# Optimization experiments

Hardware: AMD Instinct MI355X
Metric: run time of the kernel (lower is better)

The kernel has to match this reference:

```python
import jax, jax.numpy as jnp
import numpy as np
import math

D_MODEL = 1024
N_HEADS = 16
HEAD_DIM = D_MODEL // N_HEADS
SEQ = 2048
BATCH = 4
MAX_SEQ_LEN = 2048
THETA = 10000.0


def setup_inputs() -> dict:
    key = jax.random.key(0)
    ks = jax.random.split(key, 5)
    std = math.sqrt(2.0 / (D_MODEL + D_MODEL))
    x = jax.random.normal(ks[0], (BATCH, SEQ, D_MODEL), dtype=jnp.float32)
    wq = jax.random.normal(ks[1], (D_MODEL, D_MODEL), dtype=jnp.float32) * std
    wk = jax.random.normal(ks[2], (D_MODEL, D_MODEL), dtype=jnp.float32) * std
    wv = jax.random.normal(ks[3], (D_MODEL, D_MODEL), dtype=jnp.float32) * std
    wo = jax.random.normal(ks[4], (D_MODEL, D_MODEL), dtype=jnp.float32) * std
    token_positions = jnp.arange(SEQ, dtype=jnp.int32)
    return {"x": x, "token_positions": token_positions,
            "wq": wq, "wk": wk, "wv": wv, "wo": wo}


def _rope_tables(token_positions):
    # thetas_i = 1 / theta^(2i/d_k), angles[p, i] = p * thetas_i
    thetas = 1.0 / (THETA ** (2.0 * jnp.arange(HEAD_DIM // 2, dtype=jnp.float32) / HEAD_DIM))
    positions = jnp.arange(MAX_SEQ_LEN, dtype=jnp.float32)
    angles = jnp.outer(positions, thetas)  # [max_seq, d_k/2]
    cos = jnp.cos(angles)[token_positions]  # [S, d_k/2]
    sin = jnp.sin(angles)[token_positions]
    return cos, sin


def _apply_rope(x, cos, sin):
    # x: [B, H, S, D]; pairs (even, odd) form complex numbers
    shp = x.shape
    x2 = x.reshape(*shp[:-1], HEAD_DIM // 2, 2)
    xe, xo = x2[..., 0], x2[..., 1]
    re = xe * cos - xo * sin
    im = xe * sin + xo * cos
    return jnp.stack([re, im], axis=-1).reshape(shp)


def reference(x, token_positions, wq, wk, wv, wo):
    B, S, _ = x.shape
    # LinearNoBias: einsum('...j,ij->...i', x, W)
    q = jnp.einsum('bsj,ij->bsi', x, wq)
    k = jnp.einsum('bsj,ij->bsi', x, wk)
    v = jnp.einsum('bsj,ij->bsi', x, wv)
    # split heads -> [B, H, S, D]
    q = q.reshape(B, S, N_HEADS, HEAD_DIM).transpose(0, 2, 1, 3)
    k = k.reshape(B, S, N_HEADS, HEAD_DIM).transpose(0, 2, 1, 3)
    v = v.reshape(B, S, N_HEADS, HEAD_DIM).transpose(0, 2, 1, 3)
    cos, sin = _rope_tables(token_positions)
    q = _apply_rope(q, cos, sin)
    k = _apply_rope(k, cos, sin)
    scores = jnp.einsum('bhqd,bhkd->bhqk', q, k) / math.sqrt(HEAD_DIM)
    causal = jnp.tril(jnp.ones((S, S), dtype=bool))
    scores = jnp.where(causal, scores, -jnp.inf)
    probs = jax.nn.softmax(scores, axis=-1)
    out = jnp.einsum('bhqk,bhkd->bhqd', probs, v)
    out = out.transpose(0, 2, 1, 3).reshape(B, S, N_HEADS * HEAD_DIM)
    return jnp.einsum('bsj,ij->bsi', out, wo)
```

## Files before the change

### kernel.cpp

```cpp
#include <hip/hip_runtime.h>
#include <stdint.h>

#define B_SZ 4
#define S_LEN 2048
#define NH 16
#define HD 64
#define DM 1024

typedef __bf16 bf16;
typedef __bf16 bf16x4 __attribute__((ext_vector_type(4)));
typedef __bf16 bf16x8 __attribute__((ext_vector_type(8)));
typedef float f32x4 __attribute__((ext_vector_type(4)));

#define MFMA16(a, b, c) __builtin_amdgcn_mfma_f32_16x16x32_bf16(a, b, c, 0, 0, 0)

__device__ __forceinline__ void gl2lds16(const void* g, void* l) {
  __builtin_amdgcn_global_load_lds(
      (__attribute__((address_space(1))) const void*)g,
      (__attribute__((address_space(3))) void*)l, 16, 0, 0);
}

__device__ __forceinline__ void bar_lgkm() {
  asm volatile("s_waitcnt lgkmcnt(0)\n\ts_barrier" ::: "memory");
}

__device__ __forceinline__ bf16x8 ldcvt(const float* p) {
  f32x4 u0 = *(const f32x4*)p;
  f32x4 u1 = *(const f32x4*)(p + 4);
  bf16x8 v;
#pragma unroll
  for (int j = 0; j < 4; j++) {
    v[j] = (bf16)u0[j];
    v[4 + j] = (bf16)u1[j];
  }
  return v;
}

__global__ void cvt_kernel(const float* __restrict__ x,
                           const float* __restrict__ wq,
                           const float* __restrict__ wk,
                           const float* __restrict__ wv,
                           const float* __restrict__ wo,
                           bf16* __restrict__ Xb, bf16* __restrict__ Wb,
                           long xN) {
  const long e = ((long)blockIdx.x * 256 + threadIdx.x) * 8;
  const float* src;
  bf16* dst;
  long off;
  if (e < xN) {
    src = x; dst = Xb; off = e;
  } else {
    const long w = e - xN;
    const int wi = (int)(w >> 20);
    src = (wi == 0) ? wq : (wi == 1) ? wk : (wi == 2) ? wv : wo;
    dst = Wb + ((size_t)wi << 20);
    off = w & ((1L << 20) - 1);
  }
  *(bf16x8*)(dst + off) = ldcvt(src + off);
}

__device__ __forceinline__ void gemm_core_bb(const bf16* __restrict__ Ag,
                                             const bf16* __restrict__ Bg,
                                             f32x4 acc[4][4], bf16* As,
                                             bf16* Bs) {
  const int tid = threadIdx.x;
  const int lane = tid & 63;
  const int wave = tid >> 6;
  const int wm = (wave >> 1) * 64;
  const int wn = (wave & 1) * 64;
  const int col = lane & 15;
  const int kq = (lane >> 4) * 8;
  const int r0 = tid >> 2;
  const int c0 = (tid & 3) * 8;
#pragma unroll
  for (int i = 0; i < 4; i++)
#pragma unroll
    for (int j = 0; j < 4; j++) acc[i][j] = (f32x4){0.f, 0.f, 0.f, 0.f};

  for (int k0 = 0; k0 < 1024; k0 += 32) {
    __syncthreads();
    gl2lds16(Ag + (size_t)r0 * 1024 + k0 + c0, As + tid * 8);
    gl2lds16(Ag + (size_t)(r0 + 64) * 1024 + k0 + c0, As + 2048 + tid * 8);
    gl2lds16(Bg + (size_t)r0 * 1024 + k0 + c0, Bs + tid * 8);
    gl2lds16(Bg + (size_t)(r0 + 64) * 1024 + k0 + c0, Bs + 2048 + tid * 8);
    __syncthreads();

    bf16x8 af[4], bfr[4];
#pragma unroll
    for (int i = 0; i < 4; i++)
      af[i] = *(const bf16x8*)(As + (wm + i * 16 + col) * 32 + kq);
#pragma unroll
    for (int j = 0; j < 4; j++)
      bfr[j] = *(const bf16x8*)(Bs + (wn + j * 16 + col) * 32 + kq);
#pragma unroll
    for (int i = 0; i < 4; i++)
#pragma unroll
      for (int j = 0; j < 4; j++)
        acc[i][j] = MFMA16(af[i], bfr[j], acc[i][j]);
  }
}

__global__ __launch_bounds__(256, 4) void qkv_gemm(
    const bf16* __restrict__ x, const bf16* __restrict__ Wb,
    bf16* __restrict__ Q, bf16* __restrict__ K, bf16* __restrict__ Vt) {
  __shared__ __align__(16) bf16 As[128 * 32];
  __shared__ __align__(16) bf16 Bs[128 * 32];
  const int bx = blockIdx.x;
  const int by = blockIdx.y;
  const int wsel = by >> 3;
  const int n0 = (by & 7) * 128;

  f32x4 acc[4][4];
  gemm_core_bb(x + (size_t)bx * 128 * 1024,
               Wb + ((size_t)wsel << 20) + (size_t)n0 * 1024, acc, As, Bs);

  const int lane = threadIdx.x & 63;
  const int wave = threadIdx.x >> 6;
  const int wm = (wave >> 1) * 64, wn = (wave & 1) * 64;
  const int col = lane & 15, quad = lane >> 4;

  if (wsel < 2) {
    bf16* dst = wsel ? K : Q;
#pragma unroll
    for (int i = 0; i < 4; i++) {
      const int m0 = bx * 128 + wm + i * 16 + quad * 4;
#pragma unroll
      for (int j = 0; j < 4; j++) {
        const int n = n0 + wn + j * 16 + col;
        const int h = n >> 6, d = n & 63;
#pragma unroll
        for (int r = 0; r < 4; r++) {
          const int mm = m0 + r;
          const int bl = mm >> 11, s = mm & 2047;
          dst[((((size_t)bl * NH + h) * S_LEN + s) << 6) + d] =
              (bf16)acc[i][j][r];
        }
      }
    }
  } else {
#pragma unroll
    for (int i = 0; i < 4; i++) {
      const int m0 = bx * 128 + wm + i * 16 + quad * 4;
      const int bl = m0 >> 11, s = m0 & 2047;
#pragma unroll
      for (int j = 0; j < 4; j++) {
        const int n = n0 + wn + j * 16 + col;
        const int h = n >> 6, d = n & 63;
        bf16x4 pk;
#pragma unroll
        for (int r = 0; r < 4; r++) pk[r] = (bf16)acc[i][j][r];
        *(bf16x4*)(Vt + (((size_t)(bl * NH + h) * 64 + d) << 11) + s) = pk;
      }
    }
  }
}

__global__ void rope_kernel(bf16* __restrict__ q, bf16* __restrict__ k,
                            const int* __restrict__ tp) {
  const float CS = 0.18033688011112042f;
  const int idx = blockIdx.x * 256 + threadIdx.x;
  const int srow = idx >> 3;
  const int d0 = (idx & 7) * 8;
  const int s = srow & (S_LEN - 1);
  const float pf = (float)tp[s];
  const int i0 = d0 >> 1;
  float cs[4], sn[4];
#pragma unroll
  for (int j = 0; j < 4; j++) {
    float freq = __builtin_exp2f(-(float)(i0 + j) * 0.41524101186091903f);
    float ang = pf * freq;
    sincosf(ang, &sn[j], &cs[j]);
  }
  const size_t off = (size_t)srow * 64 + d0;
  bf16x8 vq = *(bf16x8*)(q + off);
  bf16x8 vk = *(bf16x8*)(k + off);
#pragma unroll
  for (int j = 0; j < 4; j++) {
    float e = (float)vq[2 * j], o = (float)vq[2 * j + 1];
    vq[2 * j] = (bf16)((e * cs[j] - o * sn[j]) * CS);
    vq[2 * j + 1] = (bf16)((e * sn[j] + o * cs[j]) * CS);
    e = (float)vk[2 * j];
    o = (float)vk[2 * j + 1];
    vk[2 * j] = (bf16)(e * cs[j] - o * sn[j]);
    vk[2 * j + 1] = (bf16)(e * sn[j] + o * cs[j]);
  }
  *(bf16x8*)(q + off) = vq;
  *(bf16x8*)(k + off) = vk;
}

#define KP 72
#define VP 136
#define PP 72
__global__ __launch_bounds__(256, 2) void attn_kernel(
    const bf16* __restrict__ Q, const bf16* __restrict__ K,
    const bf16* __restrict__ Vt, bf16* __restrict__ O) {
  __shared__ __align__(16) bf16 Ks[128 * KP];
  __shared__ __align__(16) bf16 Vts[64 * VP];
  __shared__ __align__(16) bf16 Ps[4 * 64 * PP];

  const int tid = threadIdx.x, lane = tid & 63, wave = tid >> 6;
  const int col = lane & 15, quad = lane >> 4, kq = quad * 8;
  const int bh = blockIdx.x;
  const int yb = blockIdx.y;
  const int qt = (yb < 4) ? (7 - yb) : (yb - 4);
  const int bl = bh >> 4, h = bh & 15;
  const bf16* Kg = K + (size_t)bh * S_LEN * 64;
  const bf16* Vg = Vt + (size_t)bh * 64 * S_LEN;
  bf16* Pw = Ps + wave * 64 * PP;
  const int wq_abs = qt * 256 + wave * 64;
  const int qmax = wq_abs + 63;

  const bf16* Qg = Q + ((size_t)bh * S_LEN + wq_abs) * 64;
  bf16x8 qf[4][2];
#pragma unroll
  for (int mi = 0; mi < 4; mi++)
#pragma unroll
    for (int kc = 0; kc < 2; kc++)
      qf[mi][kc] =
          *(const bf16x8*)(Qg + (mi * 16 + col) * 64 + kc * 32 + kq);

  f32x4 oacc[4][4];
  float lst[4] = {0.f, 0.f, 0.f, 0.f};
#pragma unroll
  for (int mi = 0; mi < 4; mi++)
#pragma unroll
    for (int nd = 0; nd < 4; nd++) oacc[mi][nd] = (f32x4){0.f, 0.f, 0.f, 0.f};

  const int kiters = 2 * qt + 2;
  bf16x8 kreg[4], vreg[4];
#pragma unroll
  for (int p = 0; p < 4; p++) {
    const int g = p * 256 + tid;
    kreg[p] = *(const bf16x8*)(Kg + (size_t)(g >> 3) * 64 + (g & 7) * 8);
    vreg[p] = *(const bf16x8*)(Vg + (size_t)(g >> 4) * S_LEN + (g & 15) * 8);
  }

  for (int kt = 0; kt < kiters; kt++) {
    bar_lgkm();
#pragma unroll
    for (int p = 0; p < 4; p++) {
      const int g = p * 256 + tid;
      *(bf16x8*)(Ks + (g >> 3) * KP + (g & 7) * 8) = kreg[p];
      *(bf16x8*)(Vts + (g >> 4) * VP + (g & 15) * 8) = vreg[p];
    }
    if (kt + 1 < kiters) {
#pragma unroll
      for (int p = 0; p < 4; p++) {
        const int g = p * 256 + tid;
        kreg[p] = *(const bf16x8*)(Kg + (size_t)((kt + 1) * 128 + (g >> 3)) * 64 +
                                   (g & 7) * 8);
        vreg[p] = *(const bf16x8*)(Vg + (size_t)(g >> 4) * S_LEN +
                                   (kt + 1) * 128 + (g & 15) * 8);
      }
    }
    bar_lgkm();
    if (kt * 128 > qmax) continue;

#pragma unroll
    for (int hf = 0; hf < 2; hf++) {
      const int kb = kt * 128 + hf * 64;
      if (kb > qmax) break;
      f32x4 sa[4][4];
#pragma unroll
      for (int ni = 0; ni < 4; ni++) {
        const int krow = hf * 64 + ni * 16 + col;
        bf16x8 kf0 = *(const bf16x8*)(Ks + krow * KP + kq);
        bf16x8 kf1 = *(const bf16x8*)(Ks + krow * KP + 32 + kq);
#pragma unroll
        for (int mi = 0; mi < 4; mi++) {
          f32x4 s = {0.f, 0.f, 0.f, 0.f};
          s = MFMA16(kf0, qf[mi][0], s);
          s = MFMA16(kf1, qf[mi][1], s);
          sa[mi][ni] = s;
        }
      }
      if (kb + 63 > wq_abs) {
        const int base = kb - wq_abs + quad * 4;
#pragma unroll
        for (int mi = 0; mi < 4; mi++)
#pragma unroll
          for (int ni = 0; ni < 4; ni++)
#pragma unroll
            for (int r = 0; r < 4; r++)
              if (base + ni * 16 + r > mi * 16 + col) sa[mi][ni][r] = -1e30f;
      }
#pragma unroll
      for (int mi = 0; mi < 4; mi++) {
        float rs = 0.f;
#pragma unroll
        for (int ni = 0; ni < 4; ni++)
#pragma unroll
          for (int r = 0; r < 4; r++) {
            float pv = __builtin_exp2f(sa[mi][ni][r]);
            sa[mi][ni][r] = pv;
            rs += pv;
          }
        lst[mi] += rs;
      }
#pragma unroll
      for (int mi = 0; mi < 4; mi++)
#pragma unroll
        for (int ni = 0; ni < 4; ni++) {
          bf16x4 pk;
#pragma unroll
          for (int r = 0; r < 4; r++) pk[r] = (bf16)sa[mi][ni][r];
          *(bf16x4*)(Pw + (mi * 16 + col) * PP + ni * 16 + quad * 4) = pk;
        }
#pragma unroll
      for (int kcl = 0; kcl < 2; kcl++) {
        bf16x8 pf[4];
#pragma unroll
        for (int mi = 0; mi < 4; mi++)
          pf[mi] = *(const bf16x8*)(Pw + (mi * 16 + col) * PP + kcl * 32 + kq);
#pragma unroll
        for (int nd = 0; nd < 4; nd++) {
          bf16x8 vf = *(const bf16x8*)(Vts + (nd * 16 + col) * VP + hf * 64 +
                                       kcl * 32 + kq);
#pragma unroll
          for (int mi = 0; mi < 4; mi++)
            oacc[mi][nd] = MFMA16(pf[mi], vf, oacc[mi][nd]);
        }
      }
    }
  }

#pragma unroll
  for (int mi = 0; mi < 4; mi++) {
    float rs = lst[mi];
    rs += __shfl_xor(rs, 16);
    rs += __shfl_xor(rs, 32);
    const float il = 1.0f / rs;
    float linv[4];
#pragma unroll
    for (int r = 0; r < 4; r++) linv[r] = __shfl(il, quad * 4 + r);
    const int srow0 = wq_abs + mi * 16 + quad * 4;
#pragma unroll
    for (int nd = 0; nd < 4; nd++)
#pragma unroll
      for (int r = 0; r < 4; r++)
        O[(size_t)(bl * S_LEN + srow0 + r) * DM + h * 64 + nd * 16 + col] =
            (bf16)(oacc[mi][nd][r] * linv[r]);
  }
}

__global__ __launch_bounds__(256, 4) void out_gemm(const bf16* __restrict__ A,
                                                   const bf16* __restrict__ W,
                                                   float* __restrict__ out) {
  __shared__ __align__(16) bf16 As[128 * 32];
  __shared__ __align__(16) bf16 Bs[128 * 32];
  f32x4 acc[4][4];
  gemm_core_bb(A + (size_t)blockIdx.x * 128 * 1024,
               W + (size_t)blockIdx.y * 128 * 1024, acc, As, Bs);
  const int lane = threadIdx.x & 63;
  const int wave = threadIdx.x >> 6;
  const int wm = (wave >> 1) * 64, wn = (wave & 1) * 64;
  const int col = lane & 15, quad = lane >> 4;
#pragma unroll
  for (int i = 0; i < 4; i++) {
    const int m0 = blockIdx.x * 128 + wm + i * 16 + quad * 4;
#pragma unroll
    for (int j = 0; j < 4; j++) {
      const int n = blockIdx.y * 128 + wn + j * 16 + col;
#pragma unroll
      for (int r = 0; r < 4; r++)
        out[(size_t)(m0 + r) * DM + n] = acc[i][j][r];
    }
  }
}

extern "C" void kernel_launch(void* const* d_in, const int* in_sizes, int n_in,
                              void* d_out, int out_size, void* d_ws,
                              size_t ws_size, hipStream_t stream) {
  const float* x = (const float*)d_in[0];
  const int* tp = (const int*)d_in[1];
  const float* wq = (const float*)d_in[2];
  const float* wk = (const float*)d_in[3];
  const float* wv = (const float*)d_in[4];
  const float* wo = (const float*)d_in[5];
  float* out = (float*)d_out;
  bf16* wsb = (bf16*)d_ws;

  const size_t TENb = (size_t)NH * S_LEN * HD;
  const size_t WSZ = 4ull * DM * DM;
  int bcnt = 1;
  if (ws_size >= (4 * 4 * TENb + WSZ) * sizeof(bf16)) bcnt = 4;
  else if (ws_size >= (4 * 2 * TENb + WSZ) * sizeof(bf16)) bcnt = 2;

  const size_t REG = (size_t)bcnt * TENb;
  bf16* Xb = wsb;
  bf16* Qw = wsb + REG;
  bf16* Kw = wsb + 2 * REG;
  bf16* Vtw = wsb + 3 * REG;
  bf16* Wb = wsb + 4 * REG;
  bf16* Ow = Xb;

  for (int b0 = 0; b0 < B_SZ; b0 += bcnt) {
    const float* xb = x + (size_t)b0 * S_LEN * DM;
    float* outb = out + (size_t)b0 * S_LEN * DM;
    const long cvtN = (long)(REG + WSZ);
    hipLaunchKernelGGL(cvt_kernel, dim3((unsigned)(cvtN / 2048)), dim3(256), 0,
                       stream, xb, wq, wk, wv, wo, Xb, Wb, (long)REG);
    hipLaunchKernelGGL(qkv_gemm, dim3(bcnt * 16, 24), dim3(256), 0, stream,
                       Xb, Wb, Qw, Kw, Vtw);
    hipLaunchKernelGGL(rope_kernel, dim3(bcnt * 1024), dim3(256), 0, stream,
                       Qw, Kw, tp);
    hipLaunchKernelGGL(attn_kernel, dim3(bcnt * 16, 8), dim3(256), 0, stream,
                       Qw, Kw, Vtw, Ow);
    hipLaunchKernelGGL(out_gemm, dim3(bcnt * 16, 8), dim3(256), 0, stream,
                       Ow, Wb + 3ull * DM * DM, outb);
  }
}
```

Baseline: 277.0 us.

## Load K/V fragments directly from global memory, dropping shared-memory staging and barriers

The attention kernel no longer stages K and V tiles through shared memory with block-wide barriers. Each wave now loads its K and transposed-V MFMA fragments straight from global memory (relying on L1/L2 for reuse across the four waves) and iterates only up to its own causal bound in 64-key steps. This removes the barriers and LDS traffic and lets waves proceed independently. In exchange, global/cache traffic rises fourfold since waves no longer share loads, and there is no explicit prefetching to hide latency.

Result: slower. 285.9 us (+3.2%).

```diff
diff --git a/kernel.cpp b/kernel.cpp
--- a/kernel.cpp
+++ b/kernel.cpp
@@ -18,10 +18,6 @@
   __builtin_amdgcn_global_load_lds(
       (__attribute__((address_space(1))) const void*)g,
       (__attribute__((address_space(3))) void*)l, 16, 0, 0);
-}
-
-__device__ __forceinline__ void bar_lgkm() {
-  asm volatile("s_waitcnt lgkmcnt(0)\n\ts_barrier" ::: "memory");
 }
 
 __device__ __forceinline__ bf16x8 ldcvt(const float* p) {
@@ -188,14 +184,10 @@
   *(bf16x8*)(k + off) = vk;
 }
 
-#define KP 72
-#define VP 136
 #define PP 72
 __global__ __launch_bounds__(256, 2) void attn_kernel(
     const bf16* __restrict__ Q, const bf16* __restrict__ K,
     const bf16* __restrict__ Vt, bf16* __restrict__ O) {
-  __shared__ __align__(16) bf16 Ks[128 * KP];
-  __shared__ __align__(16) bf16 Vts[64 * VP];
   __shared__ __align__(16) bf16 Ps[4 * 64 * PP];
 
   const int tid = threadIdx.x, lane = tid & 63, wave = tid >> 6;
@@ -208,7 +200,6 @@
   const bf16* Vg = Vt + (size_t)bh * 64 * S_LEN;
   bf16* Pw = Ps + wave * 64 * PP;
   const int wq_abs = qt * 256 + wave * 64;
-  const int qmax = wq_abs + 63;
 
   const bf16* Qg = Q + ((size_t)bh * S_LEN + wq_abs) * 64;
   bf16x8 qf[4][2];
@@ -226,102 +217,84 @@
 #pragma unroll
     for (int nd = 0; nd < 4; nd++) oacc[mi][nd] = (f32x4){0.f, 0.f, 0.f, 0.f};
 
-  const int kiters = 2 * qt + 2;
-  bf16x8 kreg[4], vreg[4];
-#pragma unroll
-  for (int p = 0; p < 4; p++) {
-    const int g = p * 256 + tid;
-    kreg[p] = *(const bf16x8*)(Kg + (size_t)(g >> 3) * 64 + (g & 7) * 8);
-    vreg[p] = *(const bf16x8*)(Vg + (size_t)(g >> 4) * S_LEN + (g & 15) * 8);
-  }
-
-  for (int kt = 0; kt < kiters; kt++) {
-    bar_lgkm();
-#pragma unroll
-    for (int p = 0; p < 4; p++) {
-      const int g = p * 256 + tid;
-      *(bf16x8*)(Ks + (g >> 3) * KP + (g & 7) * 8) = kreg[p];
-      *(bf16x8*)(Vts + (g >> 4) * VP + (g & 15) * 8) = vreg[p];
-    }
-    if (kt + 1 < kiters) {
-#pragma unroll
-      for (int p = 0; p < 4; p++) {
-        const int g = p * 256 + tid;
-        kreg[p] = *(const bf16x8*)(Kg + (size_t)((kt + 1) * 128 + (g >> 3)) * 64 +
-                                   (g & 7) * 8);
-        vreg[p] = *(const bf16x8*)(Vg + (size_t)(g >> 4) * S_LEN +
-                                   (kt + 1) * 128 + (g & 15) * 8);
+  for (int kb = 0; kb <= wq_abs; kb += 64) {
+    bf16x8 kf[4][2];
+#pragma unroll
+    for (int ni = 0; ni < 4; ni++)
+#pragma unroll
+      for (int kc = 0; kc < 2; kc++)
+        kf[ni][kc] = *(const bf16x8*)(Kg + (size_t)(kb + ni * 16 + col) * 64 +
+                                      kc * 32 + kq);
+    bf16x8 vf0[4];
+#pragma unroll
+    for (int nd = 0; nd < 4; nd++)
+      vf0[nd] =
+          *(const bf16x8*)(Vg + (size_t)(nd * 16 + col) * S_LEN + kb + kq);
+
+    f32x4 sa[4][4];
+#pragma unroll
+    for (int ni = 0; ni < 4; ni++)
+#pragma unroll
+      for (int mi = 0; mi < 4; mi++) {
+        f32x4 s = {0.f, 0.f, 0.f, 0.f};
+        s = MFMA16(kf[ni][0], qf[mi][0], s);
+        s = MFMA16(kf[ni][1], qf[mi][1], s);
+        sa[mi][ni] = s;
       }
-    }
-    bar_lgkm();
-    if (kt * 128 > qmax) continue;
-
-#pragma unroll
-    for (int hf = 0; hf < 2; hf++) {
-      const int kb = kt * 128 + hf * 64;
-      if (kb > qmax) break;
-      f32x4 sa[4][4];
+    if (kb == wq_abs) {
+      const int base = quad * 4;
+#pragma unroll
+      for (int mi = 0; mi < 4; mi++)
+#pragma unroll
+        for (int ni = 0; ni < 4; ni++)
+#pragma unroll
+          for (int r = 0; r < 4; r++)
+            if (base + ni * 16 + r > mi * 16 + col) sa[mi][ni][r] = -1e30f;
+    }
+#pragma unroll
+    for (int mi = 0; mi < 4; mi++) {
+      float rs = 0.f;
+#pragma unroll
+      for (int ni = 0; ni < 4; ni++)
+#pragma unroll
+        for (int r = 0; r < 4; r++) {
+          float pv = __builtin_exp2f(sa[mi][ni][r]);
+          sa[mi][ni][r] = pv;
+          rs += pv;
+        }
+      lst[mi] += rs;
+    }
+#pragma unroll
+    for (int mi = 0; mi < 4; mi++)
 #pragma unroll
       for (int ni = 0; ni < 4; ni++) {
-        const int krow = hf * 64 + ni * 16 + col;
-        bf16x8 kf0 = *(const bf16x8*)(Ks + krow * KP + kq);
-        bf16x8 kf1 = *(const bf16x8*)(Ks + krow * KP + 32 + kq);
-#pragma unroll
-        for (int mi = 0; mi < 4; mi++) {
-          f32x4 s = {0.f, 0.f, 0.f, 0.f};
-          s = MFMA16(kf0, qf[mi][0], s);
-          s = MFMA16(kf1, qf[mi][1], s);
-          sa[mi][ni] = s;
-        }
+        bf16x4 pk;
+#pragma unroll
+        for (int r = 0; r < 4; r++) pk[r] = (bf16)sa[mi][ni][r];
+        *(bf16x4*)(Pw + (mi * 16 + col) * PP + ni * 16 + quad * 4) = pk;
       }
-      if (kb + 63 > wq_abs) {
-        const int base = kb - wq_abs + quad * 4;
-#pragma unroll
-        for (int mi = 0; mi < 4; mi++)
-#pragma unroll
-          for (int ni = 0; ni < 4; ni++)
-#pragma unroll
-            for (int r = 0; r < 4; r++)
-              if (base + ni * 16 + r > mi * 16 + col) sa[mi][ni][r] = -1e30f;
-      }
-#pragma unroll
-      for (int mi = 0; mi < 4; mi++) {
-        float rs = 0.f;
-#pragma unroll
-        for (int ni = 0; ni < 4; ni++)
-#pragma unroll
-          for (int r = 0; r < 4; r++) {
-            float pv = __builtin_exp2f(sa[mi][ni][r]);
-            sa[mi][ni][r] = pv;
-            rs += pv;
-          }
-        lst[mi] += rs;
-      }
+    bf16x8 vf1[4];
+#pragma unroll
+    for (int nd = 0; nd < 4; nd++)
+      vf1[nd] = *(const bf16x8*)(Vg + (size_t)(nd * 16 + col) * S_LEN + kb +
+                                 32 + kq);
+    bf16x8 pf[4];
+#pragma unroll
+    for (int mi = 0; mi < 4; mi++)
+      pf[mi] = *(const bf16x8*)(Pw + (mi * 16 + col) * PP + kq);
+#pragma unroll
+    for (int nd = 0; nd < 4; nd++)
 #pragma unroll
       for (int mi = 0; mi < 4; mi++)
-#pragma unroll
-        for (int ni = 0; ni < 4; ni++) {
-          bf16x4 pk;
-#pragma unroll
-          for (int r = 0; r < 4; r++) pk[r] = (bf16)sa[mi][ni][r];
-          *(bf16x4*)(Pw + (mi * 16 + col) * PP + ni * 16 + quad * 4) = pk;
-        }
-#pragma unroll
-      for (int kcl = 0; kcl < 2; kcl++) {
-        bf16x8 pf[4];
-#pragma unroll
-        for (int mi = 0; mi < 4; mi++)
-          pf[mi] = *(const bf16x8*)(Pw + (mi * 16 + col) * PP + kcl * 32 + kq);
-#pragma unroll
-        for (int nd = 0; nd < 4; nd++) {
-          bf16x8 vf = *(const bf16x8*)(Vts + (nd * 16 + col) * VP + hf * 64 +
-                                       kcl * 32 + kq);
-#pragma unroll
-          for (int mi = 0; mi < 4; mi++)
-            oacc[mi][nd] = MFMA16(pf[mi], vf, oacc[mi][nd]);
-        }
-      }
-    }
+        oacc[mi][nd] = MFMA16(pf[mi], vf0[nd], oacc[mi][nd]);
+#pragma unroll
+    for (int mi = 0; mi < 4; mi++)
+      pf[mi] = *(const bf16x8*)(Pw + (mi * 16 + col) * PP + 32 + kq);
+#pragma unroll
+    for (int nd = 0; nd < 4; nd++)
+#pragma unroll
+      for (int mi = 0; mi < 4; mi++)
+        oacc[mi][nd] = MFMA16(pf[mi], vf1[nd], oacc[mi][nd]);
   }
 
 #pragma unroll
```
